# Performance work log

Measured on AMD Instinct MI355X. Metric: run time of the kernel, lower is better.

## Reference

```python
import jax, jax.numpy as jnp
import numpy as np

IN_SIZE = 4096   # input_size
OUT_SIZE = 4096  # output_size
RANK = 1024      # len(S_4), multiple of 32
GROUPSIZE = 128
BITS = 4
PACK = 32 // BITS  # 8 nibbles per int32
MAXQ_MASK = (1 << BITS) - 1  # 15


def _dequant4(qweight, qzeros, scales, g_idx):
    """GPTQ 4-bit dequant. qweight: int32 [K//8, N]; qzeros: int32 [G, N//8];
    scales: [G, N]; g_idx: int32 [K]. Returns W [K, N] with
    W[k, n] = (int4[k, n] - (zero4[g_idx[k], n] + 1)) * scales[g_idx[k], n]."""
    shifts = (jnp.arange(PACK, dtype=jnp.int32) * BITS)
    K = qweight.shape[0] * PACK
    N = qweight.shape[1]
    # unpack along rows: [K//8, 8, N] -> [K, N]
    intw = ((qweight[:, None, :] >> shifts[None, :, None]) & MAXQ_MASK).reshape(K, N)
    # unpack along cols: [G, N//8, 8] -> [G, N]; pack() stored zeros-1, so add 1 back
    zeros = ((qzeros[:, :, None] >> shifts[None, None, :]) & MAXQ_MASK).reshape(qzeros.shape[0], N) + 1
    sc = scales[g_idx]            # [K, N]
    zr = zeros[g_idx].astype(scales.dtype)  # [K, N]
    return (intw.astype(scales.dtype) - zr) * sc


def setup_inputs() -> dict:
    key = jax.random.key(0)
    ks = jax.random.split(key, 9)
    qweight_V = jax.random.randint(ks[0], (IN_SIZE // PACK, RANK), 0, 2**31 - 1, dtype=jnp.int32)
    qzeros_V = jax.random.randint(ks[1], (IN_SIZE // GROUPSIZE, RANK // PACK), 0, 2**31 - 1, dtype=jnp.int32)
    scales_V = jax.random.uniform(ks[2], (IN_SIZE // GROUPSIZE, RANK), dtype=jnp.float32) * 0.01 + 1e-3
    g_idx_V = (jnp.arange(IN_SIZE, dtype=jnp.int32) // GROUPSIZE).astype(jnp.int32)
    qweight_U = jax.random.randint(ks[3], (RANK // PACK, OUT_SIZE), 0, 2**31 - 1, dtype=jnp.int32)
    qzeros_U = jax.random.randint(ks[4], (RANK // GROUPSIZE, OUT_SIZE // PACK), 0, 2**31 - 1, dtype=jnp.int32)
    scales_U = jax.random.uniform(ks[5], (RANK // GROUPSIZE, OUT_SIZE), dtype=jnp.float32) * 0.01 + 1e-3
    g_idx_U = (jnp.arange(RANK, dtype=jnp.int32) // GROUPSIZE).astype(jnp.int32)
    S = jax.random.uniform(ks[6], (RANK,), dtype=jnp.float32) + 0.1  # singular values
    x = jax.random.normal(ks[7], (4, 2048, IN_SIZE), dtype=jnp.float32)
    return {"x": x,
            "qweight_V": qweight_V, "qzeros_V": qzeros_V, "scales_V": scales_V, "g_idx_V": g_idx_V,
            "qweight_U": qweight_U, "qzeros_U": qzeros_U, "scales_U": scales_U, "g_idx_U": g_idx_U,
            "S": S}


def reference(x, qweight_V, qzeros_V, scales_V, g_idx_V,
              qweight_U, qzeros_U, scales_U, g_idx_U, S):
    # weight_V: dequantized [IN_SIZE, RANK]; weight_U: dequantized [RANK, OUT_SIZE]
    weight_V = _dequant4(qweight_V, qzeros_V, scales_V, g_idx_V)
    weight_U = _dequant4(qweight_U, qzeros_U, scales_U, g_idx_U)
    # forward returns (weight_V @ diag(S) @ weight_U).T  -> [OUT_SIZE, IN_SIZE]
    # (the x @ W_V @ diag(S) @ W_U activation path in the source is dead code
    #  w.r.t. the returned value)
    return ((weight_V * S[None, :]) @ weight_U).T
```

## Files before the change

kernel.cpp:

```cpp
#include <hip/hip_runtime.h>

typedef __attribute__((ext_vector_type(8))) short bf16x8;
typedef __attribute__((ext_vector_type(4))) float f32x4;

__device__ __forceinline__ short f2bf(float f) {
  unsigned u = __builtin_bit_cast(unsigned, f);
  u += 0x7fffu + ((u >> 16) & 1u);
  return (short)(u >> 16);
}


__global__ __launch_bounds__(256) void dequant_fused(
    const int* __restrict__ qw_V, const int* __restrict__ qz_V,
    const float* __restrict__ sc_V, const float* __restrict__ S,
    short* __restrict__ A,
    const int* __restrict__ qw_U, const int* __restrict__ qz_U,
    const float* __restrict__ sc_U, short* __restrict__ B) {
  const int bid = blockIdx.x;
  if (bid < 2048) {
    const int t    = bid * 256 + threadIdx.x;
    const int tile = t >> 9;
    const int blk  = (t >> 6) & 7;
    const int lane = t & 63;
    const int m  = (tile >> 5) * 128 + blk * 16 + (lane & 15);
    const int r0 = (tile & 31) * 32 + ((lane >> 4) << 3);
    const int g  = m >> 7;
    const int sh = (m & 7) << 2;
    const int zw = qz_V[(g << 7) + (r0 >> 3)];
    const int*   wq  = qw_V + (m >> 3) * 1024 + r0;
    const float* scp = sc_V + (g << 10) + r0;
    const float* sp  = S + r0;
    bf16x8 res;
#pragma unroll
    for (int e = 0; e < 8; ++e) {
      int q = (wq[e] >> sh) & 15;
      int z = ((zw >> (e << 2)) & 15) + 1;
      res[e] = f2bf((float)(q - z) * scp[e] * sp[e]);
    }
    *(bf16x8*)(A + ((size_t)t << 3)) = res;
  } else {
    const int t    = (bid - 2048) * 256 + threadIdx.x;
    const int tile = t >> 10;
    const int blk  = (t >> 6) & 15;
    const int lane = t & 63;
    const int n  = (tile >> 5) * 256 + blk * 16 + (lane & 15);
    const int r0 = (tile & 31) * 32 + ((lane >> 4) << 3);
    const int w  = qw_U[(r0 >> 3) * 4096 + n];
    const int g  = r0 >> 7;
    const int zw = qz_U[(g << 9) + (n >> 3)];
    const int z  = ((zw >> ((n & 7) << 2)) & 15) + 1;
    const float s = sc_U[(g << 12) + n];
    bf16x8 res;
#pragma unroll
    for (int e = 0; e < 8; ++e) {
      int q = (w >> (e << 2)) & 15;
      res[e] = f2bf((float)(q - z) * s);
    }
    *(bf16x8*)(B + ((size_t)t << 3)) = res;
  }
}

#define GLL(g, l)                                                              \
  __builtin_amdgcn_global_load_lds(                                            \
      (const __attribute__((address_space(1))) void*)(g),                      \
      (__attribute__((address_space(3))) void*)(l), 16, 0, 0)

__global__ __launch_bounds__(256, 2) void gemm128x256(
    const short* __restrict__ A, const short* __restrict__ B,
    float* __restrict__ out) {
  __shared__ __align__(16) char lds[49152];
  const int tid  = threadIdx.x;
  const int lane = tid & 63;
  const int wid  = tid >> 6;
  const int wm   = wid >> 1;
  const int wn   = wid & 1;
  const int bid = ((blockIdx.x & 7) << 6) | (blockIdx.x >> 3);
  const int mp = bid >> 4;
  const int np = bid & 15;

  const short* gAp = A + (size_t)mp * 131072 + tid * 8;
  const short* gBp = B + (size_t)np * 262144 + tid * 8;

#define STAGE(kt) do {                                                         \
    const int bo_ = ((kt) & 1) * 24576;                                        \
    const size_t ga_ = (size_t)(kt) * 4096;                                    \
    const size_t gb_ = (size_t)(kt) * 8192;                                    \
    GLL(gAp + ga_,        lds + bo_ +         (wid << 10));                    \
    GLL(gAp + ga_ + 2048, lds + bo_ + 4096 +  (wid << 10));                    \
    GLL(gBp + gb_,        lds + bo_ + 8192 +  (wid << 10));                    \
    GLL(gBp + gb_ + 2048, lds + bo_ + 12288 + (wid << 10));                    \
    GLL(gBp + gb_ + 4096, lds + bo_ + 16384 + (wid << 10));                    \
    GLL(gBp + gb_ + 6144, lds + bo_ + 20480 + (wid << 10));                    \
  } while (0)

  const char* Ard = lds + (lane << 4);
  const char* Brd = lds + 8192 + (lane << 4);

  f32x4 acc[4][8];
#pragma unroll
  for (int i = 0; i < 4; ++i)
#pragma unroll
    for (int j = 0; j < 8; ++j) acc[i][j] = f32x4{0.f, 0.f, 0.f, 0.f};

  STAGE(0);
  STAGE(1);
  asm volatile("s_waitcnt vmcnt(6)" ::: "memory");
  __builtin_amdgcn_s_barrier();

  for (int kt = 0; kt < 32; ++kt) {
    const int bo = (kt & 1) * 24576;
    bf16x8 a[4], b[8];
#pragma unroll
    for (int i = 0; i < 4; ++i)
      a[i] = *(const bf16x8*)(Ard + bo + (((wm << 2) + i) << 10));
#pragma unroll
    for (int j = 0; j < 8; ++j)
      b[j] = *(const bf16x8*)(Brd + bo + (((wn << 3) + j) << 10));
    asm volatile("s_waitcnt lgkmcnt(0)" ::: "memory");
    __builtin_amdgcn_sched_barrier(0);
    __builtin_amdgcn_s_barrier();
    if (kt < 30) STAGE(kt + 2);
    __builtin_amdgcn_s_setprio(1);
#pragma unroll
    for (int i = 0; i < 4; ++i)
#pragma unroll
      for (int j = 0; j < 8; ++j)
        acc[i][j] = __builtin_amdgcn_mfma_f32_16x16x32_bf16(
            a[i], b[j], acc[i][j], 0, 0, 0);
    __builtin_amdgcn_s_setprio(0);
    if (kt < 30)       asm volatile("s_waitcnt vmcnt(6)" ::: "memory");
    else if (kt == 30) asm volatile("s_waitcnt vmcnt(0)" ::: "memory");
    if (kt < 31) __builtin_amdgcn_s_barrier();
  }

  const int mbase = (mp << 7) + (wm << 6) + ((lane >> 4) << 2);
  const int nbase = (np << 8) + (wn << 7) + (lane & 15);
#pragma unroll
  for (int i = 0; i < 4; ++i)
#pragma unroll
    for (int j = 0; j < 8; ++j)
      *(f32x4*)(out + (size_t)(nbase + j * 16) * 4096 + mbase + i * 16) =
          acc[i][j];
#undef STAGE
}

extern "C" void kernel_launch(void* const* d_in, const int* in_sizes, int n_in,
                              void* d_out, int out_size, void* d_ws, size_t ws_size,
                              hipStream_t stream) {
  const int*   qw_V = (const int*)d_in[1];
  const int*   qz_V = (const int*)d_in[2];
  const float* sc_V = (const float*)d_in[3];
  const int*   qw_U = (const int*)d_in[5];
  const int*   qz_U = (const int*)d_in[6];
  const float* sc_U = (const float*)d_in[7];
  const float* S    = (const float*)d_in[9];

  short* A = (short*)d_ws;
  short* B = (short*)d_ws + 4096 * 1024;
  float* out = (float*)d_out;

  dequant_fused<<<4096, 256, 0, stream>>>(qw_V, qz_V, sc_V, S, A,
                                          qw_U, qz_U, sc_U, B);
  gemm128x256<<<512, 256, 0, stream>>>(A, B, out);
}
```

Baseline: 52.15 us.

## Give each wave private LDS buffers to eliminate block barriers in GEMM

Restructures the GEMM so each wave loads its own A and B slices into a private triple-buffered LDS region, removing all workgroup barriers. LDS fragment reads are double-buffered in registers so MFMA work on one k-step overlaps loads for the next. In exchange, A and B tiles are loaded redundantly by two waves each, and the much larger LDS footprint drops occupancy to one block per CU.

Measured after the change: 66.95 us. 28.4% more time.

```diff
diff --git a/kernel.cpp b/kernel.cpp
--- a/kernel.cpp
+++ b/kernel.cpp
@@ -65,10 +65,10 @@
       (const __attribute__((address_space(1))) void*)(g),                      \
       (__attribute__((address_space(3))) void*)(l), 16, 0, 0)
 
-__global__ __launch_bounds__(256, 2) void gemm128x256(
+__global__ __launch_bounds__(256, 1) void gemm_nobar(
     const short* __restrict__ A, const short* __restrict__ B,
     float* __restrict__ out) {
-  __shared__ __align__(16) char lds[49152];
+  __shared__ __align__(16) char lds[147456];
   const int tid  = threadIdx.x;
   const int lane = tid & 63;
   const int wid  = tid >> 6;
@@ -78,23 +78,38 @@
   const int mp = bid >> 4;
   const int np = bid & 15;
 
-  const short* gAp = A + (size_t)mp * 131072 + tid * 8;
-  const short* gBp = B + (size_t)np * 262144 + tid * 8;
+  const short* gAp = A + (size_t)mp * 131072 + (size_t)(wm * 4) * 512 + lane * 8;
+  const short* gBp = B + (size_t)np * 262144 + (size_t)(wn * 8) * 512 + lane * 8;
+  char* const wl = lds + wid * 36864;
 
-#define STAGE(kt) do {                                                         \
-    const int bo_ = ((kt) & 1) * 24576;                                        \
-    const size_t ga_ = (size_t)(kt) * 4096;                                    \
-    const size_t gb_ = (size_t)(kt) * 8192;                                    \
-    GLL(gAp + ga_,        lds + bo_ +         (wid << 10));                    \
-    GLL(gAp + ga_ + 2048, lds + bo_ + 4096 +  (wid << 10));                    \
-    GLL(gBp + gb_,        lds + bo_ + 8192 +  (wid << 10));                    \
-    GLL(gBp + gb_ + 2048, lds + bo_ + 12288 + (wid << 10));                    \
-    GLL(gBp + gb_ + 4096, lds + bo_ + 16384 + (wid << 10));                    \
-    GLL(gBp + gb_ + 6144, lds + bo_ + 20480 + (wid << 10));                    \
+#define STG(t) do {                                                            \
+    char* s_ = wl + ((t) % 3) * 12288;                                         \
+    const short* a_ = gAp + (size_t)(t) * 4096;                                \
+    const short* b_ = gBp + (size_t)(t) * 8192;                                \
+    GLL(a_,         s_);          GLL(a_ + 512,  s_ + 1024);                   \
+    GLL(a_ + 1024,  s_ + 2048);   GLL(a_ + 1536, s_ + 3072);                   \
+    GLL(b_,         s_ + 4096);   GLL(b_ + 512,  s_ + 5120);                   \
+    GLL(b_ + 1024,  s_ + 6144);   GLL(b_ + 1536, s_ + 7168);                   \
+    GLL(b_ + 2048,  s_ + 8192);   GLL(b_ + 2560, s_ + 9216);                   \
+    GLL(b_ + 3072,  s_ + 10240);  GLL(b_ + 3584, s_ + 11264);                  \
   } while (0)
 
-  const char* Ard = lds + (lane << 4);
-  const char* Brd = lds + 8192 + (lane << 4);
+#define RD(dA, dB, t) do {                                                     \
+    const char* s_ = wl + ((t) % 3) * 12288 + (lane << 4);                     \
+    _Pragma("unroll")                                                          \
+    for (int i = 0; i < 4; ++i) dA[i] = *(const bf16x8*)(s_ + (i << 10));      \
+    _Pragma("unroll")                                                          \
+    for (int j = 0; j < 8; ++j) dB[j] = *(const bf16x8*)(s_ + 4096 + (j << 10)); \
+  } while (0)
+
+#define MM(aa, bb) do {                                                        \
+    _Pragma("unroll")                                                          \
+    for (int i = 0; i < 4; ++i)                                                \
+      _Pragma("unroll")                                                        \
+      for (int j = 0; j < 8; ++j)                                              \
+        acc[i][j] = __builtin_amdgcn_mfma_f32_16x16x32_bf16(                   \
+            aa[i], bb[j], acc[i][j], 0, 0, 0);                                 \
+  } while (0)
 
   f32x4 acc[4][8];
 #pragma unroll
@@ -102,35 +117,35 @@
 #pragma unroll
     for (int j = 0; j < 8; ++j) acc[i][j] = f32x4{0.f, 0.f, 0.f, 0.f};
 
-  STAGE(0);
-  STAGE(1);
-  asm volatile("s_waitcnt vmcnt(6)" ::: "memory");
-  __builtin_amdgcn_s_barrier();
+  bf16x8 aX[4], bX[8], aY[4], bY[8];
 
-  for (int kt = 0; kt < 32; ++kt) {
-    const int bo = (kt & 1) * 24576;
-    bf16x8 a[4], b[8];
-#pragma unroll
-    for (int i = 0; i < 4; ++i)
-      a[i] = *(const bf16x8*)(Ard + bo + (((wm << 2) + i) << 10));
-#pragma unroll
-    for (int j = 0; j < 8; ++j)
-      b[j] = *(const bf16x8*)(Brd + bo + (((wn << 3) + j) << 10));
-    asm volatile("s_waitcnt lgkmcnt(0)" ::: "memory");
-    __builtin_amdgcn_sched_barrier(0);
-    __builtin_amdgcn_s_barrier();
-    if (kt < 30) STAGE(kt + 2);
-    __builtin_amdgcn_s_setprio(1);
-#pragma unroll
-    for (int i = 0; i < 4; ++i)
-#pragma unroll
-      for (int j = 0; j < 8; ++j)
-        acc[i][j] = __builtin_amdgcn_mfma_f32_16x16x32_bf16(
-            a[i], b[j], acc[i][j], 0, 0, 0);
-    __builtin_amdgcn_s_setprio(0);
-    if (kt < 30)       asm volatile("s_waitcnt vmcnt(6)" ::: "memory");
-    else if (kt == 30) asm volatile("s_waitcnt vmcnt(0)" ::: "memory");
-    if (kt < 31) __builtin_amdgcn_s_barrier();
+  STG(0); STG(1); STG(2);
+  asm volatile("s_waitcnt vmcnt(24)" ::: "memory");
+  RD(aX, bX, 0);
+  asm volatile("s_waitcnt lgkmcnt(0)" ::: "memory");
+  __builtin_amdgcn_sched_barrier(0);
+
+  for (int u = 0; u < 16; ++u) {
+    const int t0 = 2 * u;
+    if (t0 <= 28) STG(t0 + 3);
+    if (t0 <= 28) asm volatile("s_waitcnt vmcnt(24)" ::: "memory");
+    else          asm volatile("s_waitcnt vmcnt(0)"  ::: "memory");
+    if (t0 <= 30) RD(aY, bY, t0 + 1);
+    MM(aX, bX);
+    if (t0 <= 30) {
+      asm volatile("s_waitcnt lgkmcnt(0)" ::: "memory");
+      __builtin_amdgcn_sched_barrier(0);
+    }
+    const int t1 = t0 + 1;
+    if (t1 <= 28) STG(t1 + 3);
+    if (t1 <= 28)      asm volatile("s_waitcnt vmcnt(24)" ::: "memory");
+    else if (t1 == 29) asm volatile("s_waitcnt vmcnt(12)" ::: "memory");
+    if (t1 <= 30) RD(aX, bX, t1 + 1);
+    MM(aY, bY);
+    if (t1 <= 30) {
+      asm volatile("s_waitcnt lgkmcnt(0)" ::: "memory");
+      __builtin_amdgcn_sched_barrier(0);
+    }
   }
 
   const int mbase = (mp << 7) + (wm << 6) + ((lane >> 4) << 2);
@@ -141,7 +156,9 @@
     for (int j = 0; j < 8; ++j)
       *(f32x4*)(out + (size_t)(nbase + j * 16) * 4096 + mbase + i * 16) =
           acc[i][j];
-#undef STAGE
+#undef STG
+#undef RD
+#undef MM
 }
 
 extern "C" void kernel_launch(void* const* d_in, const int* in_sizes, int n_in,
@@ -161,5 +178,5 @@
 
   dequant_fused<<<4096, 256, 0, stream>>>(qw_V, qz_V, sc_V, S, A,
                                           qw_U, qz_U, sc_U, B);
-  gemm128x256<<<512, 256, 0, stream>>>(A, B, out);
+  gemm_nobar<<<512, 256, 0, stream>>>(A, B, out);
 }
```
